# Optimization experiments

Measured on AMD Instinct MI355X. Metric: run time of the kernel, lower is better.

## Reference

```python
import jax, jax.numpy as jnp
import numpy as np

D_MODEL = 1024
NUM_HEADS = 16
DK = D_MODEL // NUM_HEADS


def setup_inputs() -> dict:
    key = jax.random.key(0)
    ks = jax.random.split(key, 12)
    B, S, D = 2, 2048, D_MODEL
    s = 1.0 / np.sqrt(D)
    inp = {
        "Q": jax.random.normal(ks[0], (B, S, D), jnp.float32),
        "K": jax.random.normal(ks[1], (B, S, D), jnp.float32),
        "V": jax.random.normal(ks[2], (B, S, D), jnp.float32),
        "Wq": jax.random.uniform(ks[3], (D, D), jnp.float32, -s, s),
        "bq": jax.random.uniform(ks[4], (D,), jnp.float32, -s, s),
        "Wk": jax.random.uniform(ks[5], (D, D), jnp.float32, -s, s),
        "bk": jax.random.uniform(ks[6], (D,), jnp.float32, -s, s),
        "Wv": jax.random.uniform(ks[7], (D, D), jnp.float32, -s, s),
        "bv": jax.random.uniform(ks[8], (D,), jnp.float32, -s, s),
        "Wo": jax.random.uniform(ks[9], (D, D), jnp.float32, -s, s),
        "bo": jax.random.uniform(ks[10], (D,), jnp.float32, -s, s),
    }
    return inp


def reference(Q, K, V, Wq, bq, Wk, bk, Wv, bv, Wo, bo):
    B, S, D = Q.shape
    H, dk = NUM_HEADS, DK
    # projections (torch Linear: x @ W.T + b), split heads -> [B,H,S,dk]
    q = (Q @ Wq.T + bq).reshape(B, S, H, dk).transpose(0, 2, 1, 3)
    k = (K @ Wk.T + bk).reshape(B, S, H, dk).transpose(0, 2, 1, 3)
    v = (V @ Wv.T + bv).reshape(B, S, H, dk).transpose(0, 2, 1, 3)
    scores = jnp.einsum("bhqd,bhkd->bhqk", q, k) / jnp.sqrt(jnp.asarray(dk, q.dtype))
    attn = jax.nn.softmax(scores, axis=-1)
    out = jnp.einsum("bhqk,bhkd->bhqd", attn, v)  # [B,H,S,dk]
    out = out.transpose(0, 2, 1, 3).reshape(B, S, D)
    return out @ Wo.T + bo
```

## Files before the change

kernel.cpp:

```cpp
#include <hip/hip_runtime.h>
#include <stdint.h>


#define AS1 __attribute__((address_space(1)))
#define AS3 __attribute__((address_space(3)))

typedef unsigned short u16;
typedef short s16x8 __attribute__((ext_vector_type(8)));
typedef float f32x4 __attribute__((ext_vector_type(4)));
typedef float f32x16 __attribute__((ext_vector_type(16)));
typedef u16   u16x4 __attribute__((ext_vector_type(4)));

#if defined(__has_builtin)
#if __has_builtin(__builtin_amdgcn_exp2f)
#define EXP2F(x) __builtin_amdgcn_exp2f(x)
#else
#define EXP2F(x) exp2f(x)
#endif
#else
#define EXP2F(x) exp2f(x)
#endif

__device__ __forceinline__ u16 f2b(float f) {
  union { float f; uint32_t u; } v;
  v.f = f;
  uint32_t r = (v.u + 0x7fffu + ((v.u >> 16) & 1u)) >> 16;
  return (u16)r;
}

__device__ __forceinline__ uint32_t cvtpk(float lo, float hi) {
  uint32_t r;
  asm("v_cvt_pk_bf16_f32 %0, %1, %2" : "=v"(r) : "v"(lo), "v"(hi));
  return r;
}

__device__ __forceinline__ float max3f(float a, float b, float c) {
  float r;
  asm("v_max3_f32 %0, %1, %2, %3" : "=v"(r) : "v"(a), "v"(b), "v"(c));
  return r;
}

__device__ __forceinline__ f32x4 mfma16(s16x8 a, s16x8 b, f32x4 c) {
  return __builtin_amdgcn_mfma_f32_16x16x32_bf16(a, b, c, 0, 0, 0);
}

__device__ __forceinline__ f32x16 mfma32(s16x8 a, s16x8 b, f32x16 c) {
  return __builtin_amdgcn_mfma_f32_32x32x16_bf16(a, b, c, 0, 0, 0);
}

__device__ __forceinline__ s16x8 ld_g16(const u16* p) {
  return *reinterpret_cast<const s16x8*>(p);
}

__device__ __forceinline__ void stage16(const u16* g, u16* lds_base) {
  __builtin_amdgcn_global_load_lds((const AS1 unsigned int*)g,
                                   (AS3 unsigned int*)lds_base, 16, 0, 0);
}

struct CvtArgs {
  const float* src[4];
  u16* dst[4];
  int cum[5];
};

__global__ __launch_bounds__(256) void cvt_all(CvtArgs a) {
  const int bx = blockIdx.x;
  int seg = 0;
#pragma unroll
  for (int i = 1; i < 4; ++i) seg += (bx >= a.cum[i]) ? 1 : 0;
  const int off = (bx - a.cum[seg]) * 256 + threadIdx.x;
  float4 f = reinterpret_cast<const float4*>(a.src[seg])[off];
  union { u16 u[4]; uint64_t q; } o;
  o.u[0] = f2b(f.x); o.u[1] = f2b(f.y); o.u[2] = f2b(f.z); o.u[3] = f2b(f.w);
  reinterpret_cast<uint64_t*>(a.dst[seg])[off] = o.q;
}

template <int MODE>
__global__ __launch_bounds__(256, (MODE == 0) ? 3 : 2)
void gemm_bt(const float* __restrict__ Aq,
             const float* __restrict__ Ak,
             const float* __restrict__ Av,
             const u16* __restrict__ Abf,
             const u16* __restrict__ Wbase,
             const float* __restrict__ bias0,
             const float* __restrict__ bias1,
             const float* __restrict__ bias2,
             u16* __restrict__ outb,
             u16* __restrict__ vtout,
             float* __restrict__ outf) {
  constexpr int ABUF = (MODE == 0) ? 4096 : 8192;
  __shared__ u16 As[2][ABUF];
  __shared__ u16 Bs[2][ABUF];
  const int tid = threadIdx.x;
  const int lane = tid & 63;
  const int w = tid >> 6;
  const int wr = w >> 1, wc = w & 1;

  const int bid = blockIdx.y * 8 + blockIdx.x;
  const int sw = (bid & 7) * 32 + (bid >> 3);
  const int n0 = (sw & 7) * 128;
  const int m0 = (sw >> 3) * 128;
  const int z = (MODE == 0) ? blockIdx.z : 0;
  const float QSC = 0.18033688011112042f;

  const float* Af = (MODE == 0) ? (z == 0 ? Aq : (z == 1 ? Ak : Av)) : nullptr;
  const u16* W = Wbase + (size_t)z * (1024u * 1024u);
  const float* bias = (MODE == 0) ? (z == 0 ? bias0 : (z == 1 ? bias1 : bias2)) : bias0;
  u16* ob = (MODE == 0) ? (outb + (size_t)z * (4096u * 1024u)) : nullptr;

  const int l15 = lane & 15, l4 = lane >> 4;

  f32x4 acc[4][4];
#pragma unroll
  for (int i = 0; i < 4; ++i)
#pragma unroll
    for (int j = 0; j < 4; ++j) acc[i][j] = {0.f, 0.f, 0.f, 0.f};

  if (MODE == 0) {
    const int sr2 = lane >> 2;
    const int sx2 = lane & 3;
    const float* gAf[2];
    const u16* gB[2];
#pragma unroll
    for (int j = 0; j < 2; ++j) {
      const int row = w * 32 + j * 16 + sr2;
      gAf[j] = Af + (size_t)(m0 + row) * 1024 + sx2 * 8;
      gB[j]  = W + (size_t)(n0 + row) * 1024 + sx2 * 8;
    }

    auto STAGEW = [&](int kt, u16* bbuf) {
#pragma unroll
      for (int j = 0; j < 2; ++j)
        stage16(gB[j] + kt, &bbuf[(w * 32 + j * 16) * 32]);
    };

    STAGEW(0, Bs[0]);
#pragma unroll
    for (int j = 0; j < 2; ++j) {
      float4 x0 = *(const float4*)(gAf[j]);
      float4 x1 = *(const float4*)(gAf[j] + 4);
      union { uint32_t d[4]; s16x8 v; } cv;
      cv.d[0] = cvtpk(x0.x, x0.y); cv.d[1] = cvtpk(x0.z, x0.w);
      cv.d[2] = cvtpk(x1.x, x1.y); cv.d[3] = cvtpk(x1.z, x1.w);
      *(s16x8*)&As[0][(w * 32 + j * 16) * 32 + lane * 8] = cv.v;
    }
    __syncthreads();

#pragma unroll 2
    for (int t = 0; t < 32; ++t) {
      const int cur = t & 1;
      float4 x0[2], x1[2];
      const bool more = (t + 1 < 32);
      if (more) {
        const int kt = (t + 1) * 32;
        STAGEW(kt, Bs[cur ^ 1]);
#pragma unroll
        for (int j = 0; j < 2; ++j) {
          x0[j] = *(const float4*)(gAf[j] + kt);
          x1[j] = *(const float4*)(gAf[j] + kt + 4);
        }
      }
      s16x8 af[4], bf[4];
#pragma unroll
      for (int mi = 0; mi < 4; ++mi)
        af[mi] = *(const s16x8*)&As[cur][(wr * 64 + mi * 16 + l15) * 32 + l4 * 8];
#pragma unroll
      for (int ni = 0; ni < 4; ++ni)
        bf[ni] = *(const s16x8*)&Bs[cur][(wc * 64 + ni * 16 + l15) * 32 + l4 * 8];
      __builtin_amdgcn_s_setprio(1);
#pragma unroll
      for (int mi = 0; mi < 4; ++mi)
#pragma unroll
        for (int ni = 0; ni < 4; ++ni)
          acc[mi][ni] = mfma16(af[mi], bf[ni], acc[mi][ni]);
      __builtin_amdgcn_s_setprio(0);
      if (more) {
#pragma unroll
        for (int j = 0; j < 2; ++j) {
          union { uint32_t d[4]; s16x8 v; } cv;
          cv.d[0] = cvtpk(x0[j].x, x0[j].y); cv.d[1] = cvtpk(x0[j].z, x0[j].w);
          cv.d[2] = cvtpk(x1[j].x, x1[j].y); cv.d[3] = cvtpk(x1[j].z, x1[j].w);
          *(s16x8*)&As[cur ^ 1][(w * 32 + j * 16) * 32 + lane * 8] = cv.v;
        }
      }
      __syncthreads();
    }
  } else {
    const int sr = lane >> 3;
    const int sx = lane & 7;
    const u16* gAb[4];
    const u16* gB[4];
#pragma unroll
    for (int j = 0; j < 4; ++j) {
      const int row = w * 32 + j * 8 + sr;
      const int lc = ((sx ^ (row & 7)) << 3);
      gAb[j] = Abf + (size_t)(m0 + row) * 1024 + lc;
      gB[j]  = W + (size_t)(n0 + row) * 1024 + lc;
    }
#pragma unroll
    for (int j = 0; j < 4; ++j) {
      stage16(gAb[j], &As[0][(w * 32 + j * 8) * 64]);
      stage16(gB[j], &Bs[0][(w * 32 + j * 8) * 64]);
    }
    __syncthreads();
#pragma unroll 2
    for (int t = 0; t < 16; ++t) {
      const int cur = t & 1;
      if (t + 1 < 16) {
        const int kt = (t + 1) * 64;
#pragma unroll
        for (int j = 0; j < 4; ++j) {
          stage16(gAb[j] + kt, &As[cur ^ 1][(w * 32 + j * 8) * 64]);
          stage16(gB[j] + kt, &Bs[cur ^ 1][(w * 32 + j * 8) * 64]);
        }
      }
#pragma unroll
      for (int ks = 0; ks < 2; ++ks) {
        s16x8 af[4], bf[4];
#pragma unroll
        for (int mi = 0; mi < 4; ++mi) {
          const int row = wr * 64 + mi * 16 + l15;
          const int sc_ = (((ks << 2) | l4) ^ (l15 & 7)) << 3;
          af[mi] = *(const s16x8*)&As[cur][row * 64 + sc_];
        }
#pragma unroll
        for (int ni = 0; ni < 4; ++ni) {
          const int row = wc * 64 + ni * 16 + l15;
          const int sc_ = (((ks << 2) | l4) ^ (l15 & 7)) << 3;
          bf[ni] = *(const s16x8*)&Bs[cur][row * 64 + sc_];
        }
        __builtin_amdgcn_s_setprio(1);
#pragma unroll
        for (int mi = 0; mi < 4; ++mi)
#pragma unroll
          for (int ni = 0; ni < 4; ++ni)
            acc[mi][ni] = mfma16(af[mi], bf[ni], acc[mi][ni]);
        __builtin_amdgcn_s_setprio(0);
      }
      __syncthreads();
    }
  }

#pragma unroll
  for (int ni = 0; ni < 4; ++ni) {
    const int col = n0 + wc * 64 + ni * 16 + l15;
    const float bv = bias[col];
#pragma unroll
    for (int mi = 0; mi < 4; ++mi) {
      const int row0 = m0 + wr * 64 + mi * 16 + l4 * 4;
      if (MODE == 0 && z == 2) {
        const int b = row0 >> 11, s0 = row0 & 2047;
        const int pos0 = (s0 & ~15) | ((s0 & 4) << 1) | ((s0 & 8) >> 1);
        const int h = col >> 6, d = col & 63;
        u16x4 pk = {f2b(acc[mi][ni][0] + bv), f2b(acc[mi][ni][1] + bv),
                    f2b(acc[mi][ni][2] + bv), f2b(acc[mi][ni][3] + bv)};
        *(u16x4*)&vtout[((size_t)(b * 16 + h) * 64 + d) * 2048 + pos0] = pk;
      } else {
#pragma unroll
        for (int r = 0; r < 4; ++r) {
          float val = acc[mi][ni][r] + bv;
          const int row = row0 + r;
          if (MODE == 0) {
            if (z == 0) val *= QSC;
            const int b = row >> 11, s = row & 2047;
            const int h = col >> 6, d = col & 63;
            ob[((size_t)(b * 16 + h) * 2048 + s) * 64 + d] = f2b(val);
          } else {
            outf[(size_t)row * 1024 + col] = val;
          }
        }
      }
    }
  }
}

__global__ __launch_bounds__(512, 2) void fattn(const u16* __restrict__ qp,
                                                const u16* __restrict__ kp,
                                                const u16* __restrict__ vt,
                                                u16* __restrict__ ao) {
  __shared__ u16 Kt[2][4096];
  __shared__ u16 Vt[2][4096];

  const int lane = threadIdx.x & 63;
  const int w = threadIdx.x >> 6;
  const int bh = blockIdx.y;
  const int b = bh >> 4, h = bh & 15;
  const int q0 = blockIdx.x * 256 + w * 32;
  const u16* qb = qp + (size_t)bh * (2048 * 64);
  const u16* kb = kp + (size_t)bh * (2048 * 64);
  const u16* vb = vt + (size_t)bh * (64 * 2048);
  const int l31 = lane & 31, hl = lane >> 5;
  const int x7 = l31 & 7;
  const float THR = 8.0f;

  const int srow = (w << 3) + (lane >> 3);
  const int c0 = (((lane & 7) ^ (srow & 7)) << 3);

  s16x8 qa[4];
#pragma unroll
  for (int kc = 0; kc < 4; ++kc)
    qa[kc] = ld_g16(qb + (size_t)(q0 + l31) * 64 + kc * 16 + hl * 8);

  f32x16 o[2];
  float lsum = 0.f;
  float mrun = 0.f;
#pragma unroll
  for (int r = 0; r < 16; ++r) { o[0][r] = 0.f; o[1][r] = 0.f; }

  stage16(kb + (size_t)srow * 64 + c0, &Kt[0][w * 512]);
  stage16(vb + (size_t)srow * 2048 + c0, &Vt[0][w * 512]);
  __syncthreads();

#pragma unroll 2
  for (int t = 0; t < 32; ++t) {
    const int cur = t & 1;
    if (t + 1 < 32) {
      const int kk = (t + 1) << 6;
      stage16(kb + (size_t)(kk + srow) * 64 + c0, &Kt[cur ^ 1][w * 512]);
      stage16(vb + (size_t)srow * 2048 + kk + c0, &Vt[cur ^ 1][w * 512]);
    }

    f32x16 sc[2];
#pragma unroll
    for (int r = 0; r < 16; ++r) { sc[0][r] = -mrun; sc[1][r] = -mrun; }
#pragma unroll
    for (int nk = 0; nk < 2; ++nk) {
      s16x8 kf[4];
#pragma unroll
      for (int kc = 0; kc < 4; ++kc)
        kf[kc] = *(const s16x8*)&Kt[cur][(nk * 32 + l31) * 64 +
                                         ((((kc << 1) | hl) ^ x7) << 3)];
      __builtin_amdgcn_s_setprio(1);
#pragma unroll
      for (int kc = 0; kc < 4; ++kc)
        sc[nk] = mfma32(kf[kc], qa[kc], sc[nk]);
      __builtin_amdgcn_s_setprio(0);
    }

    float m = -1e30f;
#pragma unroll
    for (int nk = 0; nk < 2; ++nk)
#pragma unroll
      for (int r = 0; r < 16; r += 2)
        m = max3f(m, sc[nk][r], sc[nk][r + 1]);
    m = fmaxf(m, __shfl_xor(m, 32));

    if (__any(m > THR)) {
      const float d = fmaxf(m, 0.f);
      mrun += d;
      const float alpha = EXP2F(-d);
      lsum *= alpha;
#pragma unroll
      for (int r = 0; r < 16; ++r) { sc[0][r] -= d; sc[1][r] -= d; }
#pragma unroll
      for (int r = 0; r < 16; ++r) {
        float ar = __shfl(alpha, (r & 3) + 8 * (r >> 2) + 4 * hl);
        o[0][r] *= ar; o[1][r] *= ar;
      }
    }

#pragma unroll
    for (int nk = 0; nk < 2; ++nk) {
      float p[16];
#pragma unroll
      for (int r = 0; r < 16; ++r) p[r] = EXP2F(sc[nk][r]);
#pragma unroll
      for (int r = 0; r < 16; ++r) lsum += p[r];
#pragma unroll
      for (int kc = 0; kc < 2; ++kc) {
        union { uint32_t d[4]; s16x8 v; } pa;
        pa.d[0] = cvtpk(p[kc * 8 + 0], p[kc * 8 + 1]);
        pa.d[1] = cvtpk(p[kc * 8 + 2], p[kc * 8 + 3]);
        pa.d[2] = cvtpk(p[kc * 8 + 4], p[kc * 8 + 5]);
        pa.d[3] = cvtpk(p[kc * 8 + 6], p[kc * 8 + 7]);
        const int chunk = nk * 4 + kc * 2 + hl;
#pragma unroll
        for (int dt = 0; dt < 2; ++dt) {
          s16x8 vf = *(const s16x8*)&Vt[cur][(dt * 32 + l31) * 64 +
                                             ((chunk ^ x7) << 3)];
          __builtin_amdgcn_s_setprio(1);
          o[dt] = mfma32(pa.v, vf, o[dt]);
          __builtin_amdgcn_s_setprio(0);
        }
      }
    }

    __syncthreads();
  }

  lsum += __shfl_xor(lsum, 32);
#pragma unroll
  for (int r = 0; r < 16; ++r) {
    const int qreg = (r & 3) + 8 * (r >> 2) + 4 * hl;
    const float inv = 1.0f / __shfl(lsum, qreg);
    const int row = b * 2048 + q0 + qreg;
#pragma unroll
    for (int dt = 0; dt < 2; ++dt)
      ao[(size_t)row * 1024 + h * 64 + dt * 32 + l31] = f2b(o[dt][r] * inv);
  }
}

extern "C" void kernel_launch(void* const* d_in, const int* in_sizes, int n_in,
                              void* d_out, int out_size, void* d_ws, size_t ws_size,
                              hipStream_t stream) {
  const float* Q  = (const float*)d_in[0];
  const float* K  = (const float*)d_in[1];
  const float* V  = (const float*)d_in[2];
  const float* Wq = (const float*)d_in[3];
  const float* bq = (const float*)d_in[4];
  const float* Wk = (const float*)d_in[5];
  const float* bk = (const float*)d_in[6];
  const float* Wv = (const float*)d_in[7];
  const float* bv = (const float*)d_in[8];
  const float* Wo = (const float*)d_in[9];
  const float* bo = (const float*)d_in[10];
  float* out = (float*)d_out;

  const size_t NI = (size_t)4096 * 1024;
  const size_t NW = (size_t)1024 * 1024;
  u16* WB  = (u16*)d_ws;
  u16* QKV = WB + 4 * NW;
  u16* VT  = QKV + 3 * NI;
  u16* AO  = VT + NI;

  CvtArgs ca;
  ca.src[0] = Wq; ca.dst[0] = WB;
  ca.src[1] = Wk; ca.dst[1] = WB + NW;
  ca.src[2] = Wv; ca.dst[2] = WB + 2 * NW;
  ca.src[3] = Wo; ca.dst[3] = WB + 3 * NW;
  ca.cum[0] = 0; ca.cum[1] = 1024; ca.cum[2] = 2048; ca.cum[3] = 3072; ca.cum[4] = 4096;
  cvt_all<<<dim3(4096), 256, 0, stream>>>(ca);

  gemm_bt<0><<<dim3(8, 32, 3), 256, 0, stream>>>(Q, K, V, nullptr, WB, bq, bk, bv,
                                                 QKV, VT, nullptr);
  fattn<<<dim3(8, 32), 512, 0, stream>>>(QKV, QKV + NI, VT, AO);
  gemm_bt<1><<<dim3(8, 32, 1), 256, 0, stream>>>(nullptr, nullptr, nullptr, AO,
                                                 WB + 3 * NW, bo, nullptr, nullptr,
                                                 nullptr, nullptr, out);
}
```

Baseline: 115.8 us.

## Prefetch fp32 A tiles two stages ahead with explicit vmcnt barriers in projection GEMM

Restructures the MODE 0 projection GEMM main loop so fp32 activation loads are issued two k-steps ahead into alternating register sets (even/odd), fully unrolled by pairs. It replaces __syncthreads with a custom barrier that waits only on partial vmcnt and uses sched_barrier to pin instruction ordering, so outstanding global loads can stay in flight across the barrier. This aims to hide global load latency behind MFMA. In exchange it uses more registers, and the exact vmcnt(4) count must match the number of outstanding loads.

```diff
diff --git a/kernel.cpp b/kernel.cpp
--- a/kernel.cpp
+++ b/kernel.cpp
@@ -20,6 +20,14 @@
 #else
 #define EXP2F(x) exp2f(x)
 #endif
+
+#define BARC(N)                                                               \
+  do {                                                                        \
+    __builtin_amdgcn_sched_barrier(0);                                        \
+    asm volatile("s_waitcnt vmcnt(" #N ") lgkmcnt(0)" ::: "memory");          \
+    __builtin_amdgcn_s_barrier();                                             \
+    __builtin_amdgcn_sched_barrier(0);                                        \
+  } while (0)
 
 __device__ __forceinline__ u16 f2b(float f) {
   union { float f; uint32_t u; } v;
@@ -134,39 +142,43 @@
         stage16(gB[j] + kt, &bbuf[(w * 32 + j * 16) * 32]);
     };
 
-    STAGEW(0, Bs[0]);
-#pragma unroll
-    for (int j = 0; j < 2; ++j) {
-      float4 x0 = *(const float4*)(gAf[j]);
-      float4 x1 = *(const float4*)(gAf[j] + 4);
-      union { uint32_t d[4]; s16x8 v; } cv;
-      cv.d[0] = cvtpk(x0.x, x0.y); cv.d[1] = cvtpk(x0.z, x0.w);
-      cv.d[2] = cvtpk(x1.x, x1.y); cv.d[3] = cvtpk(x1.z, x1.w);
-      *(s16x8*)&As[0][(w * 32 + j * 16) * 32 + lane * 8] = cv.v;
-    }
-    __syncthreads();
-
-#pragma unroll 2
-    for (int t = 0; t < 32; ++t) {
-      const int cur = t & 1;
-      float4 x0[2], x1[2];
-      const bool more = (t + 1 < 32);
-      if (more) {
-        const int kt = (t + 1) * 32;
-        STAGEW(kt, Bs[cur ^ 1]);
-#pragma unroll
-        for (int j = 0; j < 2; ++j) {
-          x0[j] = *(const float4*)(gAf[j] + kt);
-          x1[j] = *(const float4*)(gAf[j] + kt + 4);
-        }
-      }
+    float4 e0[2], e1[2], o0[2], o1[2];
+    auto ISSUE_E = [&](int kt) {
+#pragma unroll
+      for (int j = 0; j < 2; ++j) { e0[j] = *(const float4*)(gAf[j] + kt);
+                                    e1[j] = *(const float4*)(gAf[j] + kt + 4); }
+    };
+    auto ISSUE_O = [&](int kt) {
+#pragma unroll
+      for (int j = 0; j < 2; ++j) { o0[j] = *(const float4*)(gAf[j] + kt);
+                                    o1[j] = *(const float4*)(gAf[j] + kt + 4); }
+    };
+    auto CVT_E = [&](u16* abuf) {
+#pragma unroll
+      for (int j = 0; j < 2; ++j) {
+        union { uint32_t d[4]; s16x8 v; } cv;
+        cv.d[0] = cvtpk(e0[j].x, e0[j].y); cv.d[1] = cvtpk(e0[j].z, e0[j].w);
+        cv.d[2] = cvtpk(e1[j].x, e1[j].y); cv.d[3] = cvtpk(e1[j].z, e1[j].w);
+        *(s16x8*)&abuf[(w * 32 + j * 16) * 32 + lane * 8] = cv.v;
+      }
+    };
+    auto CVT_O = [&](u16* abuf) {
+#pragma unroll
+      for (int j = 0; j < 2; ++j) {
+        union { uint32_t d[4]; s16x8 v; } cv;
+        cv.d[0] = cvtpk(o0[j].x, o0[j].y); cv.d[1] = cvtpk(o0[j].z, o0[j].w);
+        cv.d[2] = cvtpk(o1[j].x, o1[j].y); cv.d[3] = cvtpk(o1[j].z, o1[j].w);
+        *(s16x8*)&abuf[(w * 32 + j * 16) * 32 + lane * 8] = cv.v;
+      }
+    };
+    auto MFMA = [&](const u16* abuf, const u16* bbuf) {
       s16x8 af[4], bf[4];
 #pragma unroll
       for (int mi = 0; mi < 4; ++mi)
-        af[mi] = *(const s16x8*)&As[cur][(wr * 64 + mi * 16 + l15) * 32 + l4 * 8];
+        af[mi] = *(const s16x8*)&abuf[(wr * 64 + mi * 16 + l15) * 32 + l4 * 8];
 #pragma unroll
       for (int ni = 0; ni < 4; ++ni)
-        bf[ni] = *(const s16x8*)&Bs[cur][(wc * 64 + ni * 16 + l15) * 32 + l4 * 8];
+        bf[ni] = *(const s16x8*)&bbuf[(wc * 64 + ni * 16 + l15) * 32 + l4 * 8];
       __builtin_amdgcn_s_setprio(1);
 #pragma unroll
       for (int mi = 0; mi < 4; ++mi)
@@ -174,17 +186,32 @@
         for (int ni = 0; ni < 4; ++ni)
           acc[mi][ni] = mfma16(af[mi], bf[ni], acc[mi][ni]);
       __builtin_amdgcn_s_setprio(0);
-      if (more) {
-#pragma unroll
-        for (int j = 0; j < 2; ++j) {
-          union { uint32_t d[4]; s16x8 v; } cv;
-          cv.d[0] = cvtpk(x0[j].x, x0[j].y); cv.d[1] = cvtpk(x0[j].z, x0[j].w);
-          cv.d[2] = cvtpk(x1[j].x, x1[j].y); cv.d[3] = cvtpk(x1[j].z, x1[j].w);
-          *(s16x8*)&As[cur ^ 1][(w * 32 + j * 16) * 32 + lane * 8] = cv.v;
-        }
-      }
-      __syncthreads();
-    }
+    };
+
+    STAGEW(0, Bs[0]);
+    ISSUE_E(0);
+    ISSUE_O(32);
+    CVT_E(As[0]);
+    BARC(4);
+
+    for (int it = 0; it < 15; ++it) {
+      const int t = 2 * it;
+      STAGEW((t + 1) * 32, Bs[1]);
+      ISSUE_E((t + 2) * 32);
+      MFMA(As[0], Bs[0]);
+      CVT_O(As[1]);
+      BARC(4);
+      STAGEW((t + 2) * 32, Bs[0]);
+      ISSUE_O((t + 3) * 32);
+      MFMA(As[1], Bs[1]);
+      CVT_E(As[0]);
+      BARC(4);
+    }
+    STAGEW(31 * 32, Bs[1]);
+    MFMA(As[0], Bs[0]);
+    CVT_O(As[1]);
+    BARC(0);
+    MFMA(As[1], Bs[1]);
   } else {
     const int sr = lane >> 3;
     const int sx = lane & 7;
```

Measured after the change: 115.2 us, median of 2. Within noise of the previous version (-0.5%).

## Load fp32 A fragments directly into registers, skipping LDS staging in QKV GEMM

Applied to the files above, without the earlier changes.

In the QKV projection GEMM, each wave now loads its own fp32 A rows straight from global memory into registers and converts them to bf16 MFMA fragments, instead of staging a converted A tile through shared memory. The plain __syncthreads is replaced by a custom barrier that waits only on the older outstanding vector loads, so the next tile's loads can stay in flight across it. This removes the LDS writes and reads for A, cuts LDS use (which may help occupancy), and shortens the barrier wait. The cost is that A is no longer shared across the waves in a row: each pair of waves now loads the same fp32 data, doubling global A traffic, and more registers are held for the prefetched data.

```diff
diff --git a/kernel.cpp b/kernel.cpp
--- a/kernel.cpp
+++ b/kernel.cpp
@@ -20,6 +20,14 @@
 #else
 #define EXP2F(x) exp2f(x)
 #endif
+
+#define BARC(N)                                                               \
+  do {                                                                        \
+    __builtin_amdgcn_sched_barrier(0);                                        \
+    asm volatile("s_waitcnt vmcnt(" #N ") lgkmcnt(0)" ::: "memory");          \
+    __builtin_amdgcn_s_barrier();                                             \
+    __builtin_amdgcn_sched_barrier(0);                                        \
+  } while (0)
 
 __device__ __forceinline__ u16 f2b(float f) {
   union { float f; uint32_t u; } v;
@@ -88,9 +96,10 @@
              u16* __restrict__ outb,
              u16* __restrict__ vtout,
              float* __restrict__ outf) {
-  constexpr int ABUF = (MODE == 0) ? 4096 : 8192;
-  __shared__ u16 As[2][ABUF];
-  __shared__ u16 Bs[2][ABUF];
+  constexpr int ASZ = (MODE == 0) ? 64 : 2 * 8192;
+  constexpr int BBUF = (MODE == 0) ? 4096 : 8192;
+  __shared__ u16 As[ASZ];
+  __shared__ u16 Bs[2][BBUF];
   const int tid = threadIdx.x;
   const int lane = tid & 63;
   const int w = tid >> 6;
@@ -117,16 +126,17 @@
     for (int j = 0; j < 4; ++j) acc[i][j] = {0.f, 0.f, 0.f, 0.f};
 
   if (MODE == 0) {
+    const float* gA[4];
+#pragma unroll
+    for (int mi = 0; mi < 4; ++mi)
+      gA[mi] = Af + (size_t)(m0 + wr * 64 + mi * 16 + l15) * 1024 + l4 * 8;
+
     const int sr2 = lane >> 2;
     const int sx2 = lane & 3;
-    const float* gAf[2];
     const u16* gB[2];
 #pragma unroll
-    for (int j = 0; j < 2; ++j) {
-      const int row = w * 32 + j * 16 + sr2;
-      gAf[j] = Af + (size_t)(m0 + row) * 1024 + sx2 * 8;
-      gB[j]  = W + (size_t)(n0 + row) * 1024 + sx2 * 8;
-    }
+    for (int j = 0; j < 2; ++j)
+      gB[j] = W + (size_t)(n0 + w * 32 + j * 16 + sr2) * 1024 + sx2 * 8;
 
     auto STAGEW = [&](int kt, u16* bbuf) {
 #pragma unroll
@@ -134,36 +144,36 @@
         stage16(gB[j] + kt, &bbuf[(w * 32 + j * 16) * 32]);
     };
 
+    float4 ar0[4], ar1[4];
+    auto ISSUE_A = [&](int kt) {
+#pragma unroll
+      for (int mi = 0; mi < 4; ++mi) {
+        ar0[mi] = *(const float4*)(gA[mi] + kt);
+        ar1[mi] = *(const float4*)(gA[mi] + kt + 4);
+      }
+    };
+
     STAGEW(0, Bs[0]);
-#pragma unroll
-    for (int j = 0; j < 2; ++j) {
-      float4 x0 = *(const float4*)(gAf[j]);
-      float4 x1 = *(const float4*)(gAf[j] + 4);
-      union { uint32_t d[4]; s16x8 v; } cv;
-      cv.d[0] = cvtpk(x0.x, x0.y); cv.d[1] = cvtpk(x0.z, x0.w);
-      cv.d[2] = cvtpk(x1.x, x1.y); cv.d[3] = cvtpk(x1.z, x1.w);
-      *(s16x8*)&As[0][(w * 32 + j * 16) * 32 + lane * 8] = cv.v;
-    }
-    __syncthreads();
+    ISSUE_A(0);
+    BARC(8);
 
 #pragma unroll 2
     for (int t = 0; t < 32; ++t) {
       const int cur = t & 1;
-      float4 x0[2], x1[2];
+      s16x8 af[4];
+#pragma unroll
+      for (int mi = 0; mi < 4; ++mi) {
+        union { uint32_t d[4]; s16x8 v; } cv;
+        cv.d[0] = cvtpk(ar0[mi].x, ar0[mi].y); cv.d[1] = cvtpk(ar0[mi].z, ar0[mi].w);
+        cv.d[2] = cvtpk(ar1[mi].x, ar1[mi].y); cv.d[3] = cvtpk(ar1[mi].z, ar1[mi].w);
+        af[mi] = cv.v;
+      }
       const bool more = (t + 1 < 32);
       if (more) {
-        const int kt = (t + 1) * 32;
-        STAGEW(kt, Bs[cur ^ 1]);
-#pragma unroll
-        for (int j = 0; j < 2; ++j) {
-          x0[j] = *(const float4*)(gAf[j] + kt);
-          x1[j] = *(const float4*)(gAf[j] + kt + 4);
-        }
-      }
-      s16x8 af[4], bf[4];
-#pragma unroll
-      for (int mi = 0; mi < 4; ++mi)
-        af[mi] = *(const s16x8*)&As[cur][(wr * 64 + mi * 16 + l15) * 32 + l4 * 8];
+        STAGEW((t + 1) * 32, Bs[cur ^ 1]);
+        ISSUE_A((t + 1) * 32);
+      }
+      s16x8 bf[4];
 #pragma unroll
       for (int ni = 0; ni < 4; ++ni)
         bf[ni] = *(const s16x8*)&Bs[cur][(wc * 64 + ni * 16 + l15) * 32 + l4 * 8];
@@ -174,16 +184,7 @@
         for (int ni = 0; ni < 4; ++ni)
           acc[mi][ni] = mfma16(af[mi], bf[ni], acc[mi][ni]);
       __builtin_amdgcn_s_setprio(0);
-      if (more) {
-#pragma unroll
-        for (int j = 0; j < 2; ++j) {
-          union { uint32_t d[4]; s16x8 v; } cv;
-          cv.d[0] = cvtpk(x0[j].x, x0[j].y); cv.d[1] = cvtpk(x0[j].z, x0[j].w);
-          cv.d[2] = cvtpk(x1[j].x, x1[j].y); cv.d[3] = cvtpk(x1[j].z, x1[j].w);
-          *(s16x8*)&As[cur ^ 1][(w * 32 + j * 16) * 32 + lane * 8] = cv.v;
-        }
-      }
-      __syncthreads();
+      if (more) BARC(8);
     }
   } else {
     const int sr = lane >> 3;
@@ -199,7 +200,7 @@
     }
 #pragma unroll
     for (int j = 0; j < 4; ++j) {
-      stage16(gAb[j], &As[0][(w * 32 + j * 8) * 64]);
+      stage16(gAb[j], &As[(w * 32 + j * 8) * 64]);
       stage16(gB[j], &Bs[0][(w * 32 + j * 8) * 64]);
     }
     __syncthreads();
@@ -210,7 +211,7 @@
         const int kt = (t + 1) * 64;
 #pragma unroll
         for (int j = 0; j < 4; ++j) {
-          stage16(gAb[j] + kt, &As[cur ^ 1][(w * 32 + j * 8) * 64]);
+          stage16(gAb[j] + kt, &As[(cur ^ 1) * 8192 + (w * 32 + j * 8) * 64]);
           stage16(gB[j] + kt, &Bs[cur ^ 1][(w * 32 + j * 8) * 64]);
         }
       }
@@ -221,7 +222,7 @@
         for (int mi = 0; mi < 4; ++mi) {
           const int row = wr * 64 + mi * 16 + l15;
           const int sc_ = (((ks << 2) | l4) ^ (l15 & 7)) << 3;
-          af[mi] = *(const s16x8*)&As[cur][row * 64 + sc_];
+          af[mi] = *(const s16x8*)&As[cur * 8192 + row * 64 + sc_];
         }
 #pragma unroll
         for (int ni = 0; ni < 4; ++ni) {
```

Measured after the change: 171.4 us. 47.9% more time.
